# Optimization experiments

Hardware: AMD Instinct MI355X
Metric: run time of the kernel (lower is better)

The kernel has to match this reference:

```python
import jax, jax.numpy as jnp
import numpy as np
from jax import lax

SIGMOID_THRESH = 0.05  # hard-coded in get_local_max_coords
KERNEL = 3             # default kernel_size


def setup_inputs() -> dict:
    key = jax.random.key(0)
    # [B, num_kps, H, W] heatmap logits from the DeepLab head
    heatmaps = jax.random.normal(key, (16, 17, 384, 384), dtype=jnp.float32)
    return {"heatmaps": heatmaps}


def reference(heatmaps):
    """CenterNet-style local-max peak extraction.

    Faithful to Heatmaps.get_local_max_coords: a pixel is a peak iff it equals
    the 3x3 max-pool of the logits AND sigmoid(logit) > 0.05. Instead of the
    data-dependent torch.nonzero + Python grouping loops (which just reshuffle
    the same information into ragged per-image/per-type lists), we return the
    dense, fixed-shape peak-score map: sigmoid(logit) at peak locations, 0
    elsewhere. The [B, K, H, W] layout already encodes the per-image (axis 0)
    and per-keypoint-type (axis 1) grouping of the original nested loops.
    """
    # 3x3 max-pool, stride 1, SAME padding (pad = kernel // 2)
    max_hm = lax.reduce_window(
        heatmaps,
        -jnp.inf,
        lax.max,
        window_dimensions=(1, 1, KERNEL, KERNEL),
        window_strides=(1, 1, 1, 1),
        padding="SAME",
    )
    prob = jax.nn.sigmoid(heatmaps)
    peak_mask = (max_hm == heatmaps) & (prob > SIGMOID_THRESH)
    return jnp.where(peak_mask, prob, jnp.zeros((), dtype=heatmaps.dtype))
```

## Files before the change

### kernel.cpp

```cpp
#include <hip/hip_runtime.h>
#include <math.h>

#define HH 384
#define WW 384
#define TW 64
#define TH 64
#define TX 6
#define TY 6
#define NIMG 272
#define IMG_STRIDE (HH * WW)
#define LDS_W 67
#define NELEM (66 * 66)
#define NLOAD 18

typedef float f4_t __attribute__((ext_vector_type(4)));

__device__ __forceinline__ float max3f(float a, float b, float c) {
    return fmaxf(fmaxf(a, b), c);
}
__device__ __forceinline__ float fast_sigmoid(float v) {
    return __fdividef(1.0f, 1.0f + __expf(-v));
}

__global__ __launch_bounds__(256) void
heatmap_peaks_kernel(const float* __restrict__ in, float* __restrict__ out) {
    __shared__ float S[66 * LDS_W];

    int tid = threadIdx.x;
    int bid = blockIdx.x;
    int txt = bid % TX;
    int tmp = bid / TX;
    int tyt = tmp % TY;
    int img = tmp / TY;
    int x0 = txt * TW;
    int y0 = tyt * TH;

    const float* ib = in + (size_t)img * IMG_STRIDE;
    const float NEG = -INFINITY;

    float va[NLOAD];
    bool  ok[NLOAD];
    int   le[NLOAD];
#pragma unroll
    for (int k = 0; k < NLOAD; ++k) {
        int e  = tid + k * 256;
        int ly = e / 66;
        int lx = e - ly * 66;
        int gx = x0 - 1 + lx;
        int gy = y0 - 1 + ly;
        bool valid = (e < NELEM) && ((unsigned)gx < (unsigned)WW)
                                 && ((unsigned)gy < (unsigned)HH);
        int cx = valid ? gx : 0;
        int cy = valid ? gy : 0;
        va[k] = ib[cy * WW + cx];
        ok[k] = valid;
        le[k] = ly * LDS_W + lx;
    }
#pragma unroll
    for (int k = 0; k < NLOAD; ++k) {
        int e = tid + k * 256;
        if (e < NELEM) S[le[k]] = ok[k] ? va[k] : NEG;
    }
    __syncthreads();

    int ctx = tid & 15;
    int cty = tid >> 4;
    int rb  = cty * 4;
    int cb  = ctx * 4;

    float vals[6][6];
#pragma unroll
    for (int c = 0; c < 6; ++c)
#pragma unroll
        for (int r = 0; r < 6; ++r)
            vals[c][r] = S[(rb + r) * LDS_W + cb + c];

    float vm[6][4];
#pragma unroll
    for (int c = 0; c < 6; ++c)
#pragma unroll
        for (int r = 0; r < 4; ++r)
            vm[c][r] = max3f(vals[c][r], vals[c][r + 1], vals[c][r + 2]);

    float* ob = out + (size_t)img * IMG_STRIDE
                    + (size_t)(y0 + rb) * WW + x0 + cb;
#pragma unroll
    for (int r = 0; r < 4; ++r) {
        f4_t o;
        float p, m, v;
        m = max3f(vm[0][r], vm[1][r], vm[2][r]); v = vals[1][r + 1];
        p = fast_sigmoid(v); o.x = (m == v && p > 0.05f) ? p : 0.0f;
        m = max3f(vm[1][r], vm[2][r], vm[3][r]); v = vals[2][r + 1];
        p = fast_sigmoid(v); o.y = (m == v && p > 0.05f) ? p : 0.0f;
        m = max3f(vm[2][r], vm[3][r], vm[4][r]); v = vals[3][r + 1];
        p = fast_sigmoid(v); o.z = (m == v && p > 0.05f) ? p : 0.0f;
        m = max3f(vm[3][r], vm[4][r], vm[5][r]); v = vals[4][r + 1];
        p = fast_sigmoid(v); o.w = (m == v && p > 0.05f) ? p : 0.0f;
        __builtin_nontemporal_store(o, (f4_t*)(ob + (size_t)r * WW));
    }
}

extern "C" void kernel_launch(void* const* d_in, const int* in_sizes, int n_in,
                              void* d_out, int out_size, void* d_ws, size_t ws_size,
                              hipStream_t stream) {
    const float* in = (const float*)d_in[0];
    float* out = (float*)d_out;
    int blocks = TX * TY * NIMG;
    heatmap_peaks_kernel<<<blocks, 256, 0, stream>>>(in, out);
}
```

Baseline: 260.8 us.

## Use persistent blocks with double-buffered LDS and vectorized float4 halo loads

Replaces the one-block-per-tile launch with a fixed grid of 1024 persistent blocks. Each block loops over tiles and prefetches the next tile's halo into registers while computing the current one from a double-buffered LDS tile. Global loads become float4 segments with a 4-wide halo on each side, and the LDS stride changes to 76. The aim is to hide load latency and cut instruction count. In exchange the block uses twice the LDS, which may reduce occupancy, and the wider halo fetches some extra bytes.

```diff
diff --git a/kernel.cpp b/kernel.cpp
--- a/kernel.cpp
+++ b/kernel.cpp
@@ -3,15 +3,14 @@
 
 #define HH 384
 #define WW 384
-#define TW 64
-#define TH 64
 #define TX 6
-#define TY 6
-#define NIMG 272
+#define NTILES 9792
 #define IMG_STRIDE (HH * WW)
-#define LDS_W 67
-#define NELEM (66 * 66)
-#define NLOAD 18
+#define LDS_STRIDE 76
+#define ROWS 66
+#define BUFSZ (ROWS * LDS_STRIDE)
+#define NSEG 1188
+#define GRID 1024
 
 typedef float f4_t __attribute__((ext_vector_type(4)));
 
@@ -22,58 +21,67 @@
     return __fdividef(1.0f, 1.0f + __expf(-v));
 }
 
-__global__ __launch_bounds__(256) void
-heatmap_peaks_kernel(const float* __restrict__ in, float* __restrict__ out) {
-    __shared__ float S[66 * LDS_W];
+__device__ __forceinline__ void issue_loads(const float* __restrict__ in,
+                                            int tile, int tid,
+                                            f4_t reg[5], bool vld[5]) {
+    int tx  = tile % TX;
+    int t2  = tile / TX;
+    int ty  = t2 % TX;
+    int img = t2 / TX;
+    const float* ib = in + (size_t)img * IMG_STRIDE;
+    int x0 = tx * 64, y0 = ty * 64;
+#pragma unroll
+    for (int k = 0; k < 5; ++k) {
+        int e   = tid + k * 256;
+        int row = e / 18;
+        int c4  = e - row * 18;
+        int gy  = y0 - 1 + row;
+        int gx  = x0 - 4 + c4 * 4;
+        bool v  = (e < NSEG) & ((unsigned)gy < (unsigned)HH)
+                             & ((unsigned)gx <= (unsigned)(WW - 4));
+        int cy = v ? gy : 0;
+        int cx = v ? gx : 0;
+        reg[k] = *(const f4_t*)(ib + (size_t)cy * WW + cx);
+        vld[k] = v;
+    }
+}
 
-    int tid = threadIdx.x;
-    int bid = blockIdx.x;
-    int txt = bid % TX;
-    int tmp = bid / TX;
-    int tyt = tmp % TY;
-    int img = tmp / TY;
-    int x0 = txt * TW;
-    int y0 = tyt * TH;
+__device__ __forceinline__ void write_lds(float* __restrict__ B, int tid,
+                                          const f4_t reg[5], const bool vld[5]) {
+    const float NEG = -INFINITY;
+    f4_t NEG4 = {NEG, NEG, NEG, NEG};
+#pragma unroll
+    for (int k = 0; k < 5; ++k) {
+        int e = tid + k * 256;
+        if (e < NSEG) {
+            int row = e / 18;
+            int c4  = e - row * 18;
+            *(f4_t*)(B + row * LDS_STRIDE + c4 * 4) = vld[k] ? reg[k] : NEG4;
+        }
+    }
+}
 
-    const float* ib = in + (size_t)img * IMG_STRIDE;
-    const float NEG = -INFINITY;
-
-    float va[NLOAD];
-    bool  ok[NLOAD];
-    int   le[NLOAD];
-#pragma unroll
-    for (int k = 0; k < NLOAD; ++k) {
-        int e  = tid + k * 256;
-        int ly = e / 66;
-        int lx = e - ly * 66;
-        int gx = x0 - 1 + lx;
-        int gy = y0 - 1 + ly;
-        bool valid = (e < NELEM) && ((unsigned)gx < (unsigned)WW)
-                                 && ((unsigned)gy < (unsigned)HH);
-        int cx = valid ? gx : 0;
-        int cy = valid ? gy : 0;
-        va[k] = ib[cy * WW + cx];
-        ok[k] = valid;
-        le[k] = ly * LDS_W + lx;
-    }
-#pragma unroll
-    for (int k = 0; k < NLOAD; ++k) {
-        int e = tid + k * 256;
-        if (e < NELEM) S[le[k]] = ok[k] ? va[k] : NEG;
-    }
-    __syncthreads();
+__device__ __forceinline__ void compute_tile(const float* __restrict__ A,
+                                             int tile, int tid,
+                                             float* __restrict__ out) {
+    int tx  = tile % TX;
+    int t2  = tile / TX;
+    int ty  = t2 % TX;
+    int img = t2 / TX;
+    int x0 = tx * 64, y0 = ty * 64;
 
     int ctx = tid & 15;
     int cty = tid >> 4;
     int rb  = cty * 4;
     int cb  = ctx * 4;
 
+    const float* Sp = A + rb * LDS_STRIDE + cb + 3;
     float vals[6][6];
 #pragma unroll
-    for (int c = 0; c < 6; ++c)
+    for (int r = 0; r < 6; ++r)
 #pragma unroll
-        for (int r = 0; r < 6; ++r)
-            vals[c][r] = S[(rb + r) * LDS_W + cb + c];
+        for (int c = 0; c < 6; ++c)
+            vals[c][r] = Sp[r * LDS_STRIDE + c];
 
     float vm[6][4];
 #pragma unroll
@@ -100,11 +108,35 @@
     }
 }
 
+__global__ __launch_bounds__(256) void
+heatmap_peaks_kernel(const float* __restrict__ in, float* __restrict__ out) {
+    __shared__ float S[2 * BUFSZ];
+    int tid = threadIdx.x;
+
+    int t = blockIdx.x;
+    f4_t reg[5]; bool vld[5];
+
+    issue_loads(in, t, tid, reg, vld);
+    write_lds(S, tid, reg, vld);
+    __syncthreads();
+
+    int buf = 0;
+    while (t < NTILES) {
+        int tn = t + GRID;
+        bool more = (tn < NTILES);
+        if (more) issue_loads(in, tn, tid, reg, vld);
+        compute_tile(S + buf * BUFSZ, t, tid, out);
+        if (more) write_lds(S + (buf ^ 1) * BUFSZ, tid, reg, vld);
+        __syncthreads();
+        buf ^= 1;
+        t = tn;
+    }
+}
+
 extern "C" void kernel_launch(void* const* d_in, const int* in_sizes, int n_in,
                               void* d_out, int out_size, void* d_ws, size_t ws_size,
                               hipStream_t stream) {
     const float* in = (const float*)d_in[0];
     float* out = (float*)d_out;
-    int blocks = TX * TY * NIMG;
-    heatmap_peaks_kernel<<<blocks, 256, 0, stream>>>(in, out);
+    heatmap_peaks_kernel<<<GRID, 256, 0, stream>>>(in, out);
 }
```

Result: slower. 271.7 us (+4.2%).
